# Performance work log

Measured on AMD Instinct MI355X. Metric: run time of the kernel, lower is better.

The kernel has to match this reference:

```python
import jax, jax.numpy as jnp
import numpy as np

L, N, E, H, D = 2048, 4, 1024, 16, 128  # seq, batch, embed, heads, proj_dim
HD = E // H                             # head_dim = 64
SIGMA = 1.0
EPS = 1e-6


def setup_inputs() -> dict:
    key = jax.random.key(0)
    ks = jax.random.split(key, 13)
    w = lambda i, shape: jax.random.normal(ks[i], shape, jnp.float32) * 0.02
    return {
        "query": jax.random.normal(ks[0], (L, N, E), jnp.float32),
        "key": jax.random.normal(ks[1], (L, N, E), jnp.float32),
        "value": jax.random.normal(ks[2], (L, N, E), jnp.float32),
        "wq": w(3, (E, E)), "bq": jnp.zeros((E,), jnp.float32),
        "wk": w(4, (E, E)), "bk": jnp.zeros((E,), jnp.float32),
        "wv": w(5, (E, E)), "bv": jnp.zeros((E,), jnp.float32),
        "wo": w(6, (E, E)), "bo": jnp.zeros((E,), jnp.float32),
        "random_matrices": SIGMA * jax.random.normal(ks[7], (H, D, HD), jnp.float32),
    }


def random_project(x, rm):
    # x: (L, N, H, HD), rm: (H, D, HD) -> phi: (N*H, L, 2D)
    scale = 1.0 / np.sqrt(2 * D).astype(np.float32)
    xn = x / jnp.maximum(jnp.linalg.norm(x, axis=-1, keepdims=True), 1e-12)
    xt = jnp.einsum('lnhe,hde->lnhd', xn, rm)
    phi = scale * jnp.concatenate([jnp.exp(xt), jnp.exp(-xt)], axis=-1)  # (L,N,H,2D)
    # faithful to torch .contiguous().view(-1, L, 2D): plain row-major reshape
    return phi.reshape(N * H, L, 2 * D)


def causal_product(phi_q, phi_k, v):
    # phi_q, phi_k: (B, L, 2D); v: (B, L, HD)
    B = phi_q.shape[0]
    def step(carry, inp):
        S, z = carry            # S: (B, 2D, HD) running kv; z: (B, 2D) running k-sum
        qk, kk, vv = inp        # (B, 2D), (B, 2D), (B, HD)
        S = S + kk[:, :, None] * vv[:, None, :]
        z = z + kk
        num = jnp.einsum('bd,bdh->bh', qk, S)
        den = jnp.einsum('bd,bd->b', qk, z)
        return (S, z), num / (den[:, None] + EPS)
    init = (jnp.zeros((B, 2 * D, HD), phi_q.dtype), jnp.zeros((B, 2 * D), phi_q.dtype))
    xs = (jnp.swapaxes(phi_q, 0, 1), jnp.swapaxes(phi_k, 0, 1), jnp.swapaxes(v, 0, 1))
    _, out = jax.lax.scan(step, init, xs)   # out: (L, B, HD)
    return jnp.swapaxes(out, 0, 1)          # (B, L, HD)


def reference(query, key, value, wq, bq, wk, bk, wv, bv, wo, bo, random_matrices):
    q = query @ wq.T + bq
    k = key @ wk.T + bk
    v = value @ wv.T + bv
    q = q.reshape(L, N, H, HD)
    k = k.reshape(L, N, H, HD)
    v = jnp.swapaxes(v.reshape(L, N * H, HD), 0, 1)   # (B=N*H, L, HD)
    phi_q = random_project(q, random_matrices)        # (B, L, 2D)
    phi_k = random_project(k, random_matrices)
    attn = causal_product(phi_q, phi_k, v)            # (B, L, HD)
    attn = jnp.swapaxes(attn, 0, 1).reshape(L, N, E)
    return attn @ wo.T + bo
```

## Files before the change

kernel.cpp:

```cpp
#include <hip/hip_runtime.h>
#include <math.h>


typedef unsigned short u16;
typedef unsigned int u32;
using f32x4v  = __attribute__((ext_vector_type(4))) float;
using f32x16v = __attribute__((ext_vector_type(16))) float;
using s16x8   = __attribute__((ext_vector_type(8))) short;

__device__ __forceinline__ float bf2f(u16 u) { return __uint_as_float(((u32)u) << 16); }
__device__ __forceinline__ u16 f2bf(float x) {
    u32 b = __float_as_uint(x);
    b += 0x7fff + ((b >> 16) & 1);
    return (u16)(b >> 16);
}
__device__ __forceinline__ u32 cvtpk(float lo, float hi) {
    u32 r;
    asm("v_cvt_pk_bf16_f32 %0, %1, %2" : "=v"(r) : "v"(lo), "v"(hi));
    return r;
}
__device__ __forceinline__ float exp2f_hw(float x) {
    float r;
    asm("v_exp_f32 %0, %1" : "=v"(r) : "v"(x));
    return r;
}
__device__ __forceinline__ void gload_lds16(const void* g, void* l) {
    __builtin_amdgcn_global_load_lds(
        (const __attribute__((address_space(1))) void*)g,
        (__attribute__((address_space(3))) void*)l, 16, 0, 0);
}

__global__ __launch_bounds__(256) void cvt_x_bf16(
    const float* __restrict__ q, const float* __restrict__ k,
    const float* __restrict__ v, u16* __restrict__ dst)
{
    const float* src = (blockIdx.y == 0) ? q : (blockIdx.y == 1) ? k : v;
    u16* d = dst + (size_t)blockIdx.y * 8388608;
    const size_t i = ((size_t)blockIdx.x * 256 + threadIdx.x) * 8;
    const float4 a = *(const float4*)(src + i);
    const float4 b = *(const float4*)(src + i + 4);
    u16 o[8] = {f2bf(a.x), f2bf(a.y), f2bf(a.z), f2bf(a.w),
                f2bf(b.x), f2bf(b.y), f2bf(b.z), f2bf(b.w)};
    *(uint4*)(d + i) = *(uint4*)o;
}

__global__ __launch_bounds__(256) void cvt_w_bf16(
    const float* __restrict__ w0, const float* __restrict__ w1,
    const float* __restrict__ w2, const float* __restrict__ w3,
    u16* __restrict__ dst)
{
    const float* src = (blockIdx.y == 0) ? w0 : (blockIdx.y == 1) ? w1
                     : (blockIdx.y == 2) ? w2 : w3;
    u16* d = dst + (size_t)blockIdx.y * 1048576;
    const size_t i = ((size_t)blockIdx.x * 256 + threadIdx.x) * 8;
    const float4 a = *(const float4*)(src + i);
    const float4 b = *(const float4*)(src + i + 4);
    u16 o[8] = {f2bf(a.x), f2bf(a.y), f2bf(a.z), f2bf(a.w),
                f2bf(b.x), f2bf(b.y), f2bf(b.z), f2bf(b.w)};
    *(uint4*)(d + i) = *(uint4*)o;
}

__global__ __launch_bounds__(256) void cvt_rm_bf16(
    const float* __restrict__ rm, u16* __restrict__ dst)
{
    const size_t i = ((size_t)blockIdx.x * 256 + threadIdx.x) * 8;
    const float4 a = *(const float4*)(rm + i);
    const float4 b = *(const float4*)(rm + i + 4);
    u16 o[8] = {f2bf(a.x), f2bf(a.y), f2bf(a.z), f2bf(a.w),
                f2bf(b.x), f2bf(b.y), f2bf(b.z), f2bf(b.w)};
    *(uint4*)(dst + i) = *(uint4*)o;
}

template<int OMODE>
__device__ __forceinline__ void gemm_body(
    const u16* __restrict__ A, const u16* __restrict__ Bw,
    const float* __restrict__ bias, void* __restrict__ Cp,
    int m0, int n0, u16* As, u16* Bs)
{
    const int t = threadIdx.x;
    const int wid = t >> 6, lane = t & 63;
    const int wr = wid >> 1, wc = wid & 1;
    const int l15 = lane & 15, l4 = lane >> 4;

    f32x4v acc[4][4];
#pragma unroll
    for (int i = 0; i < 4; ++i)
#pragma unroll
        for (int j = 0; j < 4; ++j)
#pragma unroll
            for (int e = 0; e < 4; ++e) acc[i][j][e] = 0.f;

    const int srow = wid * 32 + (lane >> 2);
    const int scol = (lane & 3) * 8;
    const u16* ga0 = A  + (size_t)(m0 + srow) * 1024 + scol;
    const u16* ga1 = ga0 + 16 * 1024;
    const u16* gb0 = Bw + (size_t)(n0 + srow) * 1024 + scol;
    const u16* gb1 = gb0 + 16 * 1024;
    u16* la0 = &As[wid * 1024];
    u16* la1 = la0 + 512;
    u16* lb0 = &Bs[wid * 1024];
    u16* lb1 = lb0 + 512;

    for (int k0 = 0; k0 < 1024; k0 += 32) {
        __syncthreads();
        gload_lds16(ga0 + k0, la0);
        gload_lds16(ga1 + k0, la1);
        gload_lds16(gb0 + k0, lb0);
        gload_lds16(gb1 + k0, lb1);
        __syncthreads();
        s16x8 af[4], bfr[4];
#pragma unroll
        for (int fi = 0; fi < 4; ++fi)
            af[fi] = *(const s16x8*)&As[(wr * 64 + fi * 16 + l15) * 32 + l4 * 8];
#pragma unroll
        for (int fj = 0; fj < 4; ++fj)
            bfr[fj] = *(const s16x8*)&Bs[(wc * 64 + fj * 16 + l15) * 32 + l4 * 8];
#pragma unroll
        for (int fi = 0; fi < 4; ++fi)
#pragma unroll
            for (int fj = 0; fj < 4; ++fj)
                acc[fi][fj] = __builtin_amdgcn_mfma_f32_16x16x32_bf16(af[fi], bfr[fj], acc[fi][fj], 0, 0, 0);
    }

    const int rl = l4 * 4, cl = l15;
    float bvals[4];
#pragma unroll
    for (int fj = 0; fj < 4; ++fj) bvals[fj] = bias[n0 + wc * 64 + fj * 16 + cl];
#pragma unroll
    for (int fi = 0; fi < 4; ++fi)
#pragma unroll
        for (int j = 0; j < 4; ++j) {
            const size_t m = m0 + wr * 64 + fi * 16 + rl + j;
#pragma unroll
            for (int fj = 0; fj < 4; ++fj) {
                const int n = n0 + wc * 64 + fj * 16 + cl;
                const float v = acc[fi][fj][j] + bvals[fj];
                if (OMODE == 0)      ((float*)Cp)[m * 1024 + n] = v;
                else if (OMODE == 1) ((u16*)Cp)[m * 1024 + n] = f2bf(v);
                else {
                    ((u16*)Cp)[((size_t)((m & 3) * 16 + (n >> 6)) * 64 + (n & 63)) * 2048 + (m >> 2)] = f2bf(v);
                }
            }
        }
}

template<int OMODE>
__global__ __launch_bounds__(256) void gemm_bf16(
    const u16* __restrict__ A, const u16* __restrict__ Bw,
    const float* __restrict__ bias, void* __restrict__ Cp)
{
    __shared__ __align__(16) u16 As[4096];
    __shared__ __align__(16) u16 Bs[4096];
    gemm_body<OMODE>(A, Bw, bias, Cp, blockIdx.x * 128, blockIdx.y * 128, As, Bs);
}

__global__ __launch_bounds__(256) void gemm_qk(
    const u16* __restrict__ xq, const u16* __restrict__ wq, const float* __restrict__ bq, u16* __restrict__ qp,
    const u16* __restrict__ xk, const u16* __restrict__ wk, const float* __restrict__ bk, u16* __restrict__ kp)
{
    __shared__ __align__(16) u16 As[4096];
    __shared__ __align__(16) u16 Bs[4096];
    const bool isq = (blockIdx.z == 0);
    gemm_body<1>(isq ? xq : xk, isq ? wq : wk, isq ? bq : bk, isq ? (void*)qp : (void*)kp,
                 blockIdx.x * 128, blockIdx.y * 128, As, Bs);
}

__global__ __launch_bounds__(256) void rand_project_mfma(
    const u16* __restrict__ QP, const u16* __restrict__ KP,
    const u16* __restrict__ RMB, u16* __restrict__ PHIQ, u16* __restrict__ PHIK)
{
    const u16* X  = (blockIdx.z == 0) ? QP : KP;
    u16* PHI      = (blockIdx.z == 0) ? PHIQ : PHIK;
    __shared__ __align__(16) u16 Xs[128 * 72];
    __shared__ __align__(16) u16 RMs[128 * 72];
    __shared__ float rsl_lds[128];
    const int h  = blockIdx.x;
    const int r0 = blockIdx.y * 128;
    const int t  = threadIdx.x;
    const int w  = t >> 6, lane = t & 63;
    const int l15 = lane & 15, l4 = lane >> 4;

    float sq[4];
#pragma unroll
    for (int i = 0; i < 4; ++i) {
        const int lin = t + i * 256;
        const int row = lin >> 3, oct = lin & 7;
        const uint4 xv = *(const uint4*)(X + (size_t)(r0 + row) * 1024 + h * 64 + oct * 8);
        *(uint4*)&Xs[row * 72 + oct * 8] = xv;
        const u16* pv = (const u16*)&xv;
        float s = 0.f;
#pragma unroll
        for (int e = 0; e < 8; ++e) { const float f = bf2f(pv[e]); s += f * f; }
        sq[i] = s;
        const uint4 rv = *(const uint4*)(RMB + (size_t)h * 8192 + lin * 8);
        *(uint4*)&RMs[row * 72 + oct * 8] = rv;
    }
#pragma unroll
    for (int i = 0; i < 4; ++i) {
        sq[i] += __shfl_xor(sq[i], 1);
        sq[i] += __shfl_xor(sq[i], 2);
        sq[i] += __shfl_xor(sq[i], 4);
        if ((t & 7) == 0)
            rsl_lds[(t >> 3) + i * 32] = 1.4426950408889634f / fmaxf(sqrtf(sq[i]), 1e-12f);
    }
    __syncthreads();

    const int wr = (w >> 1) * 64, wc = (w & 1) * 64;
    f32x4v acc[4][4];
#pragma unroll
    for (int i = 0; i < 4; ++i)
#pragma unroll
        for (int j = 0; j < 4; ++j)
#pragma unroll
            for (int e = 0; e < 4; ++e) acc[i][j][e] = 0.f;
#pragma unroll
    for (int ks = 0; ks < 2; ++ks) {
        s16x8 af[4], bfr[4];
#pragma unroll
        for (int fi = 0; fi < 4; ++fi)
            af[fi] = *(const s16x8*)&Xs[(wr + fi * 16 + l15) * 72 + ks * 32 + l4 * 8];
#pragma unroll
        for (int fj = 0; fj < 4; ++fj)
            bfr[fj] = *(const s16x8*)&RMs[(wc + fj * 16 + l15) * 72 + ks * 32 + l4 * 8];
#pragma unroll
        for (int fi = 0; fi < 4; ++fi)
#pragma unroll
            for (int fj = 0; fj < 4; ++fj)
                acc[fi][fj] = __builtin_amdgcn_mfma_f32_16x16x32_bf16(af[fi], bfr[fj], acc[fi][fj], 0, 0, 0);
    }

#pragma unroll
    for (int fi = 0; fi < 4; ++fi)
#pragma unroll
        for (int reg = 0; reg < 4; ++reg) {
            const int row = wr + fi * 16 + l4 * 4 + reg;
            const float rsl = rsl_lds[row];
            const size_t base = ((size_t)(r0 + row) * 16 + h) * 256;
#pragma unroll
            for (int fj = 0; fj < 4; ++fj) {
                const int d = wc + fj * 16 + l15;
                const float arg = acc[fi][fj][reg] * rsl;
                PHI[base + d]       = f2bf(exp2f_hw(arg - 4.f));
                PHI[base + 128 + d] = f2bf(exp2f_hw(-arg - 4.f));
            }
        }
}

__global__ __launch_bounds__(256) void chunk_state_mfma(
    const u16* __restrict__ PHIK, const u16* __restrict__ VPT, float* __restrict__ ST)
{
    __shared__ __align__(16) u16 Ks[64 * 136];
    __shared__ float zlds[16][132];
    const int b = blockIdx.x;
    const int c = blockIdx.y >> 1;
    const int dh = blockIdx.y & 1;
    const int t = threadIdx.x;
    const int wid = t >> 6, lane = t & 63;
    const int l15 = lane & 15, l4 = lane >> 4;
    const int wr = wid >> 1, wc = wid & 1;

    const size_t R0 = (size_t)b * 2048 + (size_t)c * 256;
    const int rgrp = t >> 4, d08 = (t & 15) * 8;

    float zpart[8];
#pragma unroll
    for (int i = 0; i < 8; ++i) zpart[i] = 0.f;

    f32x4v acc[2][4];
#pragma unroll
    for (int i = 0; i < 2; ++i)
#pragma unroll
        for (int j = 0; j < 4; ++j)
#pragma unroll
            for (int e = 0; e < 4; ++e) acc[i][j][e] = 0.f;

    for (int stage = 0; stage < 4; ++stage) {
        __syncthreads();
#pragma unroll
        for (int j = 0; j < 4; ++j) {
            const int r = rgrp + 16 * j;
            const uint4 v = *(const uint4*)(PHIK + (R0 + stage * 64 + r) * 256 + dh * 128 + d08);
            const int x = ((r >> 3) & 3) << 1;
            *(uint4*)&Ks[r * 136 + (((d08 >> 3) ^ x) << 3)] = v;
            const u16* pv = (const u16*)&v;
#pragma unroll
            for (int i = 0; i < 8; ++i) zpart[i] += bf2f(pv[i]);
        }
        __syncthreads();
#pragma unroll
        for (int ks = 0; ks < 2; ++ks) {
            const int xk = ((ks * 4 + l4) & 3) << 1;
            const int r0 = ks * 32 + l4 * 8;
            s16x8 af[2], bk[4];
#pragma unroll
            for (int fi = 0; fi < 2; ++fi) {
                const int h = wr * 32 + fi * 16 + l15;
                af[fi] = *(const s16x8*)(VPT + ((size_t)b * 64 + h) * 2048 + c * 256 + stage * 64 + ks * 32 + l4 * 8);
            }
#pragma unroll
            for (int fj = 0; fj < 4; ++fj) {
                const int d = wc * 64 + fj * 16 + l15;
                const int colk = (((d >> 3) ^ xk) << 3) + (d & 7);
#pragma unroll
                for (int e = 0; e < 8; ++e)
                    bk[fj][e] = (short)Ks[(r0 + e) * 136 + colk];
            }
#pragma unroll
            for (int fi = 0; fi < 2; ++fi)
#pragma unroll
                for (int fj = 0; fj < 4; ++fj)
                    acc[fi][fj] = __builtin_amdgcn_mfma_f32_16x16x32_bf16(af[fi], bk[fj], acc[fi][fj], 0, 0, 0);
        }
    }
    __syncthreads();
    *(float4*)&zlds[rgrp][d08]     = *(float4*)&zpart[0];
    *(float4*)&zlds[rgrp][d08 + 4] = *(float4*)&zpart[4];
    __syncthreads();
    float* st = ST + (size_t)(b * 8 + c) * 16640;
    if (t < 128) {
        float z = 0.f;
#pragma unroll
        for (int g = 0; g < 16; ++g) z += zlds[g][t];
        st[16384 + dh * 128 + t] = z;
    }
#pragma unroll
    for (int fi = 0; fi < 2; ++fi)
#pragma unroll
        for (int reg = 0; reg < 4; ++reg) {
            const int h = wr * 32 + fi * 16 + l4 * 4 + reg;
#pragma unroll
            for (int fj = 0; fj < 4; ++fj) {
                const int d = dh * 128 + wc * 64 + fj * 16 + l15;
                st[(size_t)h * 256 + d] = acc[fi][fj][reg];
            }
        }
}

__global__ void prefix_scan(const float* __restrict__ ST, u16* __restrict__ STBF)
{
    const int b = blockIdx.x;
    const int e = blockIdx.y * 256 + threadIdx.x;
    if (e >= 16640) return;
    const size_t base = (size_t)b * 8 * 16640 + e;
    float run = 0.f;
#pragma unroll
    for (int c = 0; c < 8; ++c) {
        const float v = ST[base + (size_t)c * 16640];
        STBF[(size_t)(b * 8 + c) * 16640 + e] = f2bf(run);
        run += v;
    }
}

__global__ __launch_bounds__(128) void causal_fused(
    const u16* __restrict__ PHIQ, const u16* __restrict__ PHIK,
    const u16* __restrict__ VPT, const u16* __restrict__ STBF,
    u16* __restrict__ ATT)
{
    const u32 bid = blockIdx.x;
    const int pair = (int)((bid >> 3) & 3);
    const int G  = (int)((bid >> 5) * 8 + (bid & 7));
    const int b  = G & 63;
    const int c  = G >> 6;
    const int w  = threadIdx.x >> 6;
    const int rf = w ? (7 - pair) : pair;
    const int ri = rf >> 1, fi = rf & 1;
    const int lane = threadIdx.x & 63;
    const int l31 = lane & 31, s = lane >> 5;
    const size_t chunk0 = (size_t)b * 2048 + (size_t)c * 256;
    const u16* stb = STBF + (size_t)(b * 8 + c) * 16640;

    const int qc = ri * 64 + fi * 32 + l31;
    s16x8 qf[16];
    const u16* qp = PHIQ + (chunk0 + qc) * 256 + s * 8;
#pragma unroll
    for (int ds = 0; ds < 16; ++ds)
        qf[ds] = *(const s16x8*)(qp + ds * 16);

    f32x16v o[2], o2;
#pragma unroll
    for (int e = 0; e < 16; ++e) { o[0][e] = 0.f; o[1][e] = 0.f; o2[e] = 0.f; }
    float den = 0.f;

#pragma unroll
    for (int ds = 0; ds < 16; ++ds) {
        const s16x8 zf = *(const s16x8*)(stb + 16384 + ds * 16 + s * 8);
        o2 = __builtin_amdgcn_mfma_f32_32x32x16_bf16(qf[ds], zf, o2, 0, 0, 0);
#pragma unroll
        for (int fh = 0; fh < 2; ++fh) {
            const s16x8 sx = *(const s16x8*)(stb + (fh * 32 + l31) * 256 + ds * 16 + s * 8);
            o[fh] = __builtin_amdgcn_mfma_f32_32x32x16_bf16(qf[ds], sx, o[fh], 0, 0, 0);
        }
    }

    const int kbmax = ri * 2 + fi;
    for (int kb = 0; kb <= kbmax; ++kb) {
        s16x8 vf[2][2];
#pragma unroll
        for (int kh = 0; kh < 2; ++kh)
#pragma unroll
            for (int fh = 0; fh < 2; ++fh)
                vf[kh][fh] = *(const s16x8*)(VPT + ((size_t)b * 64 + fh * 32 + l31) * 2048
                                             + c * 256 + kb * 32 + kh * 16 + s * 8);
        f32x16v p0, p1;
#pragma unroll
        for (int e = 0; e < 16; ++e) { p0[e] = 0.f; p1[e] = 0.f; }
        const u16* kptr = PHIK + (chunk0 + kb * 32 + l31) * 256 + s * 8;
#pragma unroll
        for (int ds = 0; ds < 8; ++ds) {
            const s16x8 kf0 = *(const s16x8*)(kptr + (2 * ds) * 16);
            const s16x8 kf1 = *(const s16x8*)(kptr + (2 * ds + 1) * 16);
            p0 = __builtin_amdgcn_mfma_f32_32x32x16_bf16(kf0, qf[2 * ds],     p0, 0, 0, 0);
            p1 = __builtin_amdgcn_mfma_f32_32x32x16_bf16(kf1, qf[2 * ds + 1], p1, 0, 0, 0);
        }
        f32x16v p;
#pragma unroll
        for (int e = 0; e < 16; ++e) p[e] = p0[e] + p1[e];

        const bool diag = (kb == kbmax);
        float rsum = 0.f;
#pragma unroll
        for (int reg = 0; reg < 16; ++reg) {
            if (diag) {
                const int kc = kb * 32 + (reg & 3) + 8 * (reg >> 2) + 4 * s;
                if (kc > qc) p[reg] = 0.f;
            }
            rsum += p[reg];
        }
        den += rsum;
#pragma unroll
        for (int kh = 0; kh < 2; ++kh) {
            const u32 pA_lo = cvtpk(p[8*kh + 0], p[8*kh + 1]);
            const u32 pA_hi = cvtpk(p[8*kh + 2], p[8*kh + 3]);
            const u32 pB_lo = cvtpk(p[8*kh + 4], p[8*kh + 5]);
            const u32 pB_hi = cvtpk(p[8*kh + 6], p[8*kh + 7]);
            const u32 X_lo = s ? pB_lo : pA_lo;
            const u32 X_hi = s ? pB_hi : pA_hi;
            const u32 Y_lo = s ? pA_lo : pB_lo;
            const u32 Y_hi = s ? pA_hi : pB_hi;
            const u32 sY_lo = __shfl_xor((int)Y_lo, 32);
            const u32 sY_hi = __shfl_xor((int)Y_hi, 32);
            u32 wq[4];
            wq[0] = s ? sY_lo : X_lo;
            wq[1] = s ? sY_hi : X_hi;
            wq[2] = s ? X_lo : sY_lo;
            wq[3] = s ? X_hi : sY_hi;
            s16x8 pa;
#pragma unroll
            for (int i = 0; i < 4; ++i) {
                pa[2*i]   = (short)(wq[i] & 0xffff);
                pa[2*i+1] = (short)(wq[i] >> 16);
            }
            o[0] = __builtin_amdgcn_mfma_f32_32x32x16_bf16(pa, vf[kh][0], o[0], 0, 0, 0);
            o[1] = __builtin_amdgcn_mfma_f32_32x32x16_bf16(pa, vf[kh][1], o[1], 0, 0, 0);
        }
    }

    const float denT = den + __shfl_xor(den, 32);
#pragma unroll
    for (int reg = 0; reg < 16; ++reg) {
        const int q32 = (reg & 3) + 8 * (reg >> 2) + 4 * s;
        const float dv = o2[reg] + __shfl(denT, q32);
        const float inv = 1.f / (dv + 1e-6f);
        const int qrow = c * 256 + ri * 64 + fi * 32 + q32;
        const size_t abase = (size_t)qrow * 4096 + b * 64;
        ATT[abase + l31]      = f2bf(o[0][reg] * inv);
        ATT[abase + 32 + l31] = f2bf(o[1][reg] * inv);
    }
}

extern "C" void kernel_launch(void* const* d_in, const int* in_sizes, int n_in,
                              void* d_out, int out_size, void* d_ws, size_t ws_size,
                              hipStream_t stream)
{
    const float* query = (const float*)d_in[0];
    const float* key   = (const float*)d_in[1];
    const float* value = (const float*)d_in[2];
    const float* wq    = (const float*)d_in[3];
    const float* bq    = (const float*)d_in[4];
    const float* wk    = (const float*)d_in[5];
    const float* bk    = (const float*)d_in[6];
    const float* wv    = (const float*)d_in[7];
    const float* bv    = (const float*)d_in[8];
    const float* wo    = (const float*)d_in[9];
    const float* bo    = (const float*)d_in[10];
    const float* rm    = (const float*)d_in[11];
    float* out = (float*)d_out;

    char* base = (char*)d_ws;
    u16*   phiq = (u16*)(base);
    u16*   phik = (u16*)(base +  67108864);
    u16*   qp   = (u16*)(base + 134217728);
    u16*   vpt  = (u16*)(base + 134217728);
    u16*   kp   = (u16*)(base + 150994944);
    u16*   stbf = (u16*)(base + 150994944);
    u16*   xbf  = (u16*)(base + 168034304);
    float* st   = (float*)(base + 168034304);
    u16*   attn = (u16*)(base + 168034304);
    u16*   wbf  = (u16*)(base + 218365952);
    u16*   rmb  = (u16*)(base + 226754560);

    u16* xq = xbf;
    u16* xk = xbf +  8388608;
    u16* xv = xbf + 16777216;
    u16* wqb = wbf;
    u16* wkb = wbf + 1048576;
    u16* wvb = wbf + 2097152;
    u16* wob = wbf + 3145728;

    const dim3 blk(256);
    cvt_x_bf16<<<dim3(4096, 3), blk, 0, stream>>>(query, key, value, xbf);
    cvt_w_bf16<<<dim3(512, 4), blk, 0, stream>>>(wq, wk, wv, wo, wbf);
    cvt_rm_bf16<<<dim3(64), blk, 0, stream>>>(rm, rmb);
    gemm_qk<<<dim3(64, 8, 2), blk, 0, stream>>>(xq, wqb, bq, qp, xk, wkb, bk, kp);
    rand_project_mfma<<<dim3(16, 64, 2), blk, 0, stream>>>(qp, kp, rmb, phiq, phik);
    gemm_bf16<2><<<dim3(64, 8), blk, 0, stream>>>(xv, wvb, bv, vpt);
    chunk_state_mfma<<<dim3(64, 16), blk, 0, stream>>>(phik, vpt, st);
    prefix_scan<<<dim3(64, 65), blk, 0, stream>>>(st, stbf);
    causal_fused<<<dim3(2048), dim3(128), 0, stream>>>(phiq, phik, vpt, stbf, attn);
    gemm_bf16<0><<<dim3(64, 8), blk, 0, stream>>>(attn, wob, bo, out);
}
```

Before: 291.3 us.

## Fuse input bf16 conversion into QKV GEMM and specialize causal intra-chunk loop

Drops the separate fp32-to-bf16 pass over the activations. The merged Q/K/V projection GEMM now reads fp32 inputs, converts them in registers and stores them to a swizzled LDS tile, and the V projection joins the same launch. The weight and random-matrix conversions are merged into one launch. Chunk states are stored as bf16 instead of fp32 to halve prefix-scan traffic, at some cost in precision. The causal kernel templates its intra-chunk loop on the block count so it fully unrolls, adds s_setprio around the MFMA sections, and sets a waves-per-EU launch bound.

```diff
diff --git a/kernel.cpp b/kernel.cpp
--- a/kernel.cpp
+++ b/kernel.cpp
@@ -30,12 +30,21 @@
         (__attribute__((address_space(3))) void*)l, 16, 0, 0);
 }
 
-__global__ __launch_bounds__(256) void cvt_x_bf16(
-    const float* __restrict__ q, const float* __restrict__ k,
-    const float* __restrict__ v, u16* __restrict__ dst)
-{
-    const float* src = (blockIdx.y == 0) ? q : (blockIdx.y == 1) ? k : v;
-    u16* d = dst + (size_t)blockIdx.y * 8388608;
+__global__ __launch_bounds__(256) void cvt_consts(
+    const float* __restrict__ w0, const float* __restrict__ w1,
+    const float* __restrict__ w2, const float* __restrict__ w3,
+    const float* __restrict__ rm, u16* __restrict__ wbf, u16* __restrict__ rmb)
+{
+    const int y = blockIdx.y;
+    const float* src;
+    u16* d;
+    if (y == 4) {
+        if (blockIdx.x >= 64) return;
+        src = rm; d = rmb;
+    } else {
+        src = (y == 0) ? w0 : (y == 1) ? w1 : (y == 2) ? w2 : w3;
+        d = wbf + (size_t)y * 1048576;
+    }
     const size_t i = ((size_t)blockIdx.x * 256 + threadIdx.x) * 8;
     const float4 a = *(const float4*)(src + i);
     const float4 b = *(const float4*)(src + i + 4);
@@ -44,40 +53,107 @@
     *(uint4*)(d + i) = *(uint4*)o;
 }
 
-__global__ __launch_bounds__(256) void cvt_w_bf16(
-    const float* __restrict__ w0, const float* __restrict__ w1,
-    const float* __restrict__ w2, const float* __restrict__ w3,
-    u16* __restrict__ dst)
-{
-    const float* src = (blockIdx.y == 0) ? w0 : (blockIdx.y == 1) ? w1
-                     : (blockIdx.y == 2) ? w2 : w3;
-    u16* d = dst + (size_t)blockIdx.y * 1048576;
-    const size_t i = ((size_t)blockIdx.x * 256 + threadIdx.x) * 8;
-    const float4 a = *(const float4*)(src + i);
-    const float4 b = *(const float4*)(src + i + 4);
-    u16 o[8] = {f2bf(a.x), f2bf(a.y), f2bf(a.z), f2bf(a.w),
-                f2bf(b.x), f2bf(b.y), f2bf(b.z), f2bf(b.w)};
-    *(uint4*)(d + i) = *(uint4*)o;
-}
-
-__global__ __launch_bounds__(256) void cvt_rm_bf16(
-    const float* __restrict__ rm, u16* __restrict__ dst)
-{
-    const size_t i = ((size_t)blockIdx.x * 256 + threadIdx.x) * 8;
-    const float4 a = *(const float4*)(rm + i);
-    const float4 b = *(const float4*)(rm + i + 4);
-    u16 o[8] = {f2bf(a.x), f2bf(a.y), f2bf(a.z), f2bf(a.w),
-                f2bf(b.x), f2bf(b.y), f2bf(b.z), f2bf(b.w)};
-    *(uint4*)(dst + i) = *(uint4*)o;
-}
-
-template<int OMODE>
-__device__ __forceinline__ void gemm_body(
+__global__ __launch_bounds__(256) void gemm_qkv(
+    const float* __restrict__ Xq, const float* __restrict__ Xk, const float* __restrict__ Xv,
+    const u16* __restrict__ WB, const float* __restrict__ bq, const float* __restrict__ bk,
+    const float* __restrict__ bv, u16* __restrict__ qp, u16* __restrict__ kp, u16* __restrict__ vpt)
+{
+    __shared__ __align__(16) u16 As[4096];
+    __shared__ __align__(16) u16 Bs[4096];
+    const int z = blockIdx.z;
+    const float* A = (z == 0) ? Xq : (z == 1) ? Xk : Xv;
+    const u16* Bw = WB + (size_t)z * 1048576;
+    const float* bias = (z == 0) ? bq : (z == 1) ? bk : bv;
+
+    const int t = threadIdx.x;
+    const int m0 = blockIdx.x * 128, n0 = blockIdx.y * 128;
+    const int wid = t >> 6, lane = t & 63;
+    const int wr = wid >> 1, wc = wid & 1;
+    const int l15 = lane & 15, l4 = lane >> 4;
+
+    f32x4v acc[4][4];
+#pragma unroll
+    for (int i = 0; i < 4; ++i)
+#pragma unroll
+        for (int j = 0; j < 4; ++j)
+#pragma unroll
+            for (int e = 0; e < 4; ++e) acc[i][j][e] = 0.f;
+
+    const int srow = t >> 1;
+    const int scol = (t & 1) * 16;
+    const int sx   = (srow >> 1) & 3;
+    const int sl0  = (t & 1) * 2;
+    u16* wa0 = &As[srow * 32 + ((sl0     ^ sx)) * 8];
+    u16* wa1 = &As[srow * 32 + (((sl0+1) ^ sx)) * 8];
+    const float* gsrcA = A + (size_t)(m0 + srow) * 1024 + scol;
+    const int brow = wid * 32 + (lane >> 2);
+    const int bcol = (lane & 3) * 8;
+    const u16* gb0 = Bw + (size_t)(n0 + brow) * 1024 + bcol;
+    const u16* gb1 = gb0 + 16 * 1024;
+    u16* lb0 = &Bs[wid * 1024];
+    u16* lb1 = lb0 + 512;
+
+    for (int k0 = 0; k0 < 1024; k0 += 32) {
+        __syncthreads();
+        gload_lds16(gb0 + k0, lb0);
+        gload_lds16(gb1 + k0, lb1);
+        {
+            u16 ta[16];
+#pragma unroll
+            for (int q = 0; q < 4; ++q) {
+                const float4 v = *(const float4*)(gsrcA + k0 + q * 4);
+                ta[q*4+0] = f2bf(v.x); ta[q*4+1] = f2bf(v.y);
+                ta[q*4+2] = f2bf(v.z); ta[q*4+3] = f2bf(v.w);
+            }
+            *(uint4*)wa0 = *(const uint4*)&ta[0];
+            *(uint4*)wa1 = *(const uint4*)&ta[8];
+        }
+        __syncthreads();
+        s16x8 af[4], bfr[4];
+#pragma unroll
+        for (int fi = 0; fi < 4; ++fi) {
+            const int r  = wr * 64 + fi * 16 + l15;
+            const int sl = l4 ^ ((r >> 1) & 3);
+            af[fi] = *(const s16x8*)&As[r * 32 + sl * 8];
+        }
+#pragma unroll
+        for (int fj = 0; fj < 4; ++fj)
+            bfr[fj] = *(const s16x8*)&Bs[(wc * 64 + fj * 16 + l15) * 32 + l4 * 8];
+#pragma unroll
+        for (int fi = 0; fi < 4; ++fi)
+#pragma unroll
+            for (int fj = 0; fj < 4; ++fj)
+                acc[fi][fj] = __builtin_amdgcn_mfma_f32_16x16x32_bf16(af[fi], bfr[fj], acc[fi][fj], 0, 0, 0);
+    }
+
+    u16* Cp = (z == 0) ? qp : (z == 1) ? kp : vpt;
+    const int rl = l4 * 4, cl = l15;
+    float bvals[4];
+#pragma unroll
+    for (int fj = 0; fj < 4; ++fj) bvals[fj] = bias[n0 + wc * 64 + fj * 16 + cl];
+#pragma unroll
+    for (int fi = 0; fi < 4; ++fi)
+#pragma unroll
+        for (int j = 0; j < 4; ++j) {
+            const size_t m = m0 + wr * 64 + fi * 16 + rl + j;
+#pragma unroll
+            for (int fj = 0; fj < 4; ++fj) {
+                const int n = n0 + wc * 64 + fj * 16 + cl;
+                const float v = acc[fi][fj][j] + bvals[fj];
+                if (z < 2) Cp[m * 1024 + n] = f2bf(v);
+                else       Cp[((size_t)((m & 3) * 16 + (n >> 6)) * 64 + (n & 63)) * 2048 + (m >> 2)] = f2bf(v);
+            }
+        }
+}
+
+__global__ __launch_bounds__(256) void gemm_o(
     const u16* __restrict__ A, const u16* __restrict__ Bw,
-    const float* __restrict__ bias, void* __restrict__ Cp,
-    int m0, int n0, u16* As, u16* Bs)
-{
+    const float* __restrict__ bias, float* __restrict__ Cp)
+{
+    __shared__ __align__(16) u16 As[4096];
+    __shared__ __align__(16) u16 Bs[4096];
     const int t = threadIdx.x;
+    const int m0 = blockIdx.x * 128, n0 = blockIdx.y * 128;
     const int wid = t >> 6, lane = t & 63;
     const int wr = wid >> 1, wc = wid & 1;
     const int l15 = lane & 15, l4 = lane >> 4;
@@ -134,35 +210,9 @@
 #pragma unroll
             for (int fj = 0; fj < 4; ++fj) {
                 const int n = n0 + wc * 64 + fj * 16 + cl;
-                const float v = acc[fi][fj][j] + bvals[fj];
-                if (OMODE == 0)      ((float*)Cp)[m * 1024 + n] = v;
-                else if (OMODE == 1) ((u16*)Cp)[m * 1024 + n] = f2bf(v);
-                else {
-                    ((u16*)Cp)[((size_t)((m & 3) * 16 + (n >> 6)) * 64 + (n & 63)) * 2048 + (m >> 2)] = f2bf(v);
-                }
-            }
-        }
-}
-
-template<int OMODE>
-__global__ __launch_bounds__(256) void gemm_bf16(
-    const u16* __restrict__ A, const u16* __restrict__ Bw,
-    const float* __restrict__ bias, void* __restrict__ Cp)
-{
-    __shared__ __align__(16) u16 As[4096];
-    __shared__ __align__(16) u16 Bs[4096];
-    gemm_body<OMODE>(A, Bw, bias, Cp, blockIdx.x * 128, blockIdx.y * 128, As, Bs);
-}
-
-__global__ __launch_bounds__(256) void gemm_qk(
-    const u16* __restrict__ xq, const u16* __restrict__ wq, const float* __restrict__ bq, u16* __restrict__ qp,
-    const u16* __restrict__ xk, const u16* __restrict__ wk, const float* __restrict__ bk, u16* __restrict__ kp)
-{
-    __shared__ __align__(16) u16 As[4096];
-    __shared__ __align__(16) u16 Bs[4096];
-    const bool isq = (blockIdx.z == 0);
-    gemm_body<1>(isq ? xq : xk, isq ? wq : wk, isq ? bq : bk, isq ? (void*)qp : (void*)kp,
-                 blockIdx.x * 128, blockIdx.y * 128, As, Bs);
+                Cp[m * 1024 + n] = acc[fi][fj][j] + bvals[fj];
+            }
+        }
 }
 
 __global__ __launch_bounds__(256) void rand_project_mfma(
@@ -247,7 +297,7 @@
 }
 
 __global__ __launch_bounds__(256) void chunk_state_mfma(
-    const u16* __restrict__ PHIK, const u16* __restrict__ VPT, float* __restrict__ ST)
+    const u16* __restrict__ PHIK, const u16* __restrict__ VPT, u16* __restrict__ STC)
 {
     __shared__ __align__(16) u16 Ks[64 * 136];
     __shared__ float zlds[16][132];
@@ -316,12 +366,12 @@
     *(float4*)&zlds[rgrp][d08]     = *(float4*)&zpart[0];
     *(float4*)&zlds[rgrp][d08 + 4] = *(float4*)&zpart[4];
     __syncthreads();
-    float* st = ST + (size_t)(b * 8 + c) * 16640;
+    u16* st = STC + (size_t)(b * 8 + c) * 16640;
     if (t < 128) {
         float z = 0.f;
 #pragma unroll
         for (int g = 0; g < 16; ++g) z += zlds[g][t];
-        st[16384 + dh * 128 + t] = z;
+        st[16384 + dh * 128 + t] = f2bf(z);
     }
 #pragma unroll
     for (int fi = 0; fi < 2; ++fi)
@@ -331,80 +381,46 @@
 #pragma unroll
             for (int fj = 0; fj < 4; ++fj) {
                 const int d = dh * 128 + wc * 64 + fj * 16 + l15;
-                st[(size_t)h * 256 + d] = acc[fi][fj][reg];
-            }
-        }
-}
-
-__global__ void prefix_scan(const float* __restrict__ ST, u16* __restrict__ STBF)
+                st[(size_t)h * 256 + d] = f2bf(acc[fi][fj][reg]);
+            }
+        }
+}
+
+__global__ void prefix_scan(const u16* __restrict__ STC, u16* __restrict__ STBF)
 {
     const int b = blockIdx.x;
     const int e = blockIdx.y * 256 + threadIdx.x;
     if (e >= 16640) return;
-    const size_t base = (size_t)b * 8 * 16640 + e;
     float run = 0.f;
 #pragma unroll
     for (int c = 0; c < 8; ++c) {
-        const float v = ST[base + (size_t)c * 16640];
-        STBF[(size_t)(b * 8 + c) * 16640 + e] = f2bf(run);
+        const size_t idx = (size_t)(b * 8 + c) * 16640 + e;
+        const float v = bf2f(STC[idx]);
+        STBF[idx] = f2bf(run);
         run += v;
     }
 }
 
-__global__ __launch_bounds__(128) void causal_fused(
-    const u16* __restrict__ PHIQ, const u16* __restrict__ PHIK,
-    const u16* __restrict__ VPT, const u16* __restrict__ STBF,
-    u16* __restrict__ ATT)
-{
-    const u32 bid = blockIdx.x;
-    const int pair = (int)((bid >> 3) & 3);
-    const int G  = (int)((bid >> 5) * 8 + (bid & 7));
-    const int b  = G & 63;
-    const int c  = G >> 6;
-    const int w  = threadIdx.x >> 6;
-    const int rf = w ? (7 - pair) : pair;
-    const int ri = rf >> 1, fi = rf & 1;
-    const int lane = threadIdx.x & 63;
-    const int l31 = lane & 31, s = lane >> 5;
-    const size_t chunk0 = (size_t)b * 2048 + (size_t)c * 256;
-    const u16* stb = STBF + (size_t)(b * 8 + c) * 16640;
-
-    const int qc = ri * 64 + fi * 32 + l31;
-    s16x8 qf[16];
-    const u16* qp = PHIQ + (chunk0 + qc) * 256 + s * 8;
-#pragma unroll
-    for (int ds = 0; ds < 16; ++ds)
-        qf[ds] = *(const s16x8*)(qp + ds * 16);
-
-    f32x16v o[2], o2;
-#pragma unroll
-    for (int e = 0; e < 16; ++e) { o[0][e] = 0.f; o[1][e] = 0.f; o2[e] = 0.f; }
-    float den = 0.f;
-
-#pragma unroll
-    for (int ds = 0; ds < 16; ++ds) {
-        const s16x8 zf = *(const s16x8*)(stb + 16384 + ds * 16 + s * 8);
-        o2 = __builtin_amdgcn_mfma_f32_32x32x16_bf16(qf[ds], zf, o2, 0, 0, 0);
-#pragma unroll
-        for (int fh = 0; fh < 2; ++fh) {
-            const s16x8 sx = *(const s16x8*)(stb + (fh * 32 + l31) * 256 + ds * 16 + s * 8);
-            o[fh] = __builtin_amdgcn_mfma_f32_32x32x16_bf16(qf[ds], sx, o[fh], 0, 0, 0);
-        }
-    }
-
-    const int kbmax = ri * 2 + fi;
-    for (int kb = 0; kb <= kbmax; ++kb) {
+template<int KBMAX>
+__device__ __forceinline__ void intra_unit(
+    const u16* __restrict__ kbase, const u16* __restrict__ vbase,
+    const s16x8 (&qf)[16], int qc, int l31, int s,
+    f32x16v& o0, f32x16v& o1, float& den)
+{
+#pragma unroll
+    for (int kb = 0; kb <= KBMAX; ++kb) {
         s16x8 vf[2][2];
 #pragma unroll
         for (int kh = 0; kh < 2; ++kh)
 #pragma unroll
             for (int fh = 0; fh < 2; ++fh)
-                vf[kh][fh] = *(const s16x8*)(VPT + ((size_t)b * 64 + fh * 32 + l31) * 2048
-                                             + c * 256 + kb * 32 + kh * 16 + s * 8);
+                vf[kh][fh] = *(const s16x8*)(vbase + (size_t)(fh * 32 + l31) * 2048
+                                             + kb * 32 + kh * 16 + s * 8);
         f32x16v p0, p1;
 #pragma unroll
         for (int e = 0; e < 16; ++e) { p0[e] = 0.f; p1[e] = 0.f; }
-        const u16* kptr = PHIK + (chunk0 + kb * 32 + l31) * 256 + s * 8;
+        const u16* kptr = kbase + (size_t)(kb * 32 + l31) * 256 + s * 8;
+        __builtin_amdgcn_s_setprio(1);
 #pragma unroll
         for (int ds = 0; ds < 8; ++ds) {
             const s16x8 kf0 = *(const s16x8*)(kptr + (2 * ds) * 16);
@@ -412,11 +428,12 @@
             p0 = __builtin_amdgcn_mfma_f32_32x32x16_bf16(kf0, qf[2 * ds],     p0, 0, 0, 0);
             p1 = __builtin_amdgcn_mfma_f32_32x32x16_bf16(kf1, qf[2 * ds + 1], p1, 0, 0, 0);
         }
+        __builtin_amdgcn_s_setprio(0);
         f32x16v p;
 #pragma unroll
         for (int e = 0; e < 16; ++e) p[e] = p0[e] + p1[e];
 
-        const bool diag = (kb == kbmax);
+        const bool diag = (kb == KBMAX);
         float rsum = 0.f;
 #pragma unroll
         for (int reg = 0; reg < 16; ++reg) {
@@ -450,9 +467,67 @@
                 pa[2*i]   = (short)(wq[i] & 0xffff);
                 pa[2*i+1] = (short)(wq[i] >> 16);
             }
-            o[0] = __builtin_amdgcn_mfma_f32_32x32x16_bf16(pa, vf[kh][0], o[0], 0, 0, 0);
-            o[1] = __builtin_amdgcn_mfma_f32_32x32x16_bf16(pa, vf[kh][1], o[1], 0, 0, 0);
-        }
+            __builtin_amdgcn_s_setprio(1);
+            o0 = __builtin_amdgcn_mfma_f32_32x32x16_bf16(pa, vf[kh][0], o0, 0, 0, 0);
+            o1 = __builtin_amdgcn_mfma_f32_32x32x16_bf16(pa, vf[kh][1], o1, 0, 0, 0);
+            __builtin_amdgcn_s_setprio(0);
+        }
+    }
+}
+
+__global__ __launch_bounds__(128, 3) void causal_fused(
+    const u16* __restrict__ PHIQ, const u16* __restrict__ PHIK,
+    const u16* __restrict__ VPT, const u16* __restrict__ STBF,
+    u16* __restrict__ ATT)
+{
+    const u32 bid = blockIdx.x;
+    const int pair = (int)((bid >> 3) & 3);
+    const int G  = (int)((bid >> 5) * 8 + (bid & 7));
+    const int b  = G & 63;
+    const int c  = G >> 6;
+    const int w  = threadIdx.x >> 6;
+    const int rf = w ? (7 - pair) : pair;
+    const int ri = rf >> 1, fi = rf & 1;
+    const int lane = threadIdx.x & 63;
+    const int l31 = lane & 31, s = lane >> 5;
+    const size_t chunk0 = (size_t)b * 2048 + (size_t)c * 256;
+    const u16* stb = STBF + (size_t)(b * 8 + c) * 16640;
+
+    const int qc = ri * 64 + fi * 32 + l31;
+    s16x8 qf[16];
+    const u16* qp = PHIQ + (chunk0 + qc) * 256 + s * 8;
+#pragma unroll
+    for (int ds = 0; ds < 16; ++ds)
+        qf[ds] = *(const s16x8*)(qp + ds * 16);
+
+    f32x16v o[2], o2;
+#pragma unroll
+    for (int e = 0; e < 16; ++e) { o[0][e] = 0.f; o[1][e] = 0.f; o2[e] = 0.f; }
+    float den = 0.f;
+
+#pragma unroll
+    for (int ds = 0; ds < 16; ++ds) {
+        const s16x8 zf = *(const s16x8*)(stb + 16384 + ds * 16 + s * 8);
+        o2 = __builtin_amdgcn_mfma_f32_32x32x16_bf16(qf[ds], zf, o2, 0, 0, 0);
+#pragma unroll
+        for (int fh = 0; fh < 2; ++fh) {
+            const s16x8 sx = *(const s16x8*)(stb + (fh * 32 + l31) * 256 + ds * 16 + s * 8);
+            o[fh] = __builtin_amdgcn_mfma_f32_32x32x16_bf16(qf[ds], sx, o[fh], 0, 0, 0);
+        }
+    }
+
+    const u16* kbase = PHIK + chunk0 * 256;
+    const u16* vbase = VPT + (size_t)b * 64 * 2048 + c * 256;
+    const int kbmax = ri * 2 + fi;
+    switch (kbmax) {
+        case 0: intra_unit<0>(kbase, vbase, qf, qc, l31, s, o[0], o[1], den); break;
+        case 1: intra_unit<1>(kbase, vbase, qf, qc, l31, s, o[0], o[1], den); break;
+        case 2: intra_unit<2>(kbase, vbase, qf, qc, l31, s, o[0], o[1], den); break;
+        case 3: intra_unit<3>(kbase, vbase, qf, qc, l31, s, o[0], o[1], den); break;
+        case 4: intra_unit<4>(kbase, vbase, qf, qc, l31, s, o[0], o[1], den); break;
+        case 5: intra_unit<5>(kbase, vbase, qf, qc, l31, s, o[0], o[1], den); break;
+        case 6: intra_unit<6>(kbase, vbase, qf, qc, l31, s, o[0], o[1], den); break;
+        default: intra_unit<7>(kbase, vbase, qf, qc, l31, s, o[0], o[1], den); break;
     }
 
     const float denT = den + __shfl_xor(den, 32);
@@ -487,35 +562,28 @@
     float* out = (float*)d_out;
 
     char* base = (char*)d_ws;
-    u16*   phiq = (u16*)(base);
-    u16*   phik = (u16*)(base +  67108864);
-    u16*   qp   = (u16*)(base + 134217728);
-    u16*   vpt  = (u16*)(base + 134217728);
-    u16*   kp   = (u16*)(base + 150994944);
-    u16*   stbf = (u16*)(base + 150994944);
-    u16*   xbf  = (u16*)(base + 168034304);
-    float* st   = (float*)(base + 168034304);
-    u16*   attn = (u16*)(base + 168034304);
-    u16*   wbf  = (u16*)(base + 218365952);
-    u16*   rmb  = (u16*)(base + 226754560);
-
-    u16* xq = xbf;
-    u16* xk = xbf +  8388608;
-    u16* xv = xbf + 16777216;
+    u16* phiq = (u16*)(base);
+    u16* phik = (u16*)(base +  67108864);
+    u16* vpt  = (u16*)(base + 134217728);
+    u16* stbf = (u16*)(base + 150994944);
+    u16* qp   = (u16*)(base + 168034304);
+    u16* kp   = (u16*)(base + 184811520);
+    u16* stc  = (u16*)(base + 201588736);
+    u16* wbf  = (u16*)(base + 218628096);
+    u16* rmb  = (u16*)(base + 227016704);
+    u16* attn = qp;
+
     u16* wqb = wbf;
     u16* wkb = wbf + 1048576;
     u16* wvb = wbf + 2097152;
     u16* wob = wbf + 3145728;
 
     const dim3 blk(256);
-    cvt_x_bf16<<<dim3(4096, 3), blk, 0, stream>>>(query, key, value, xbf);
-    cvt_w_bf16<<<dim3(512, 4), blk, 0, stream>>>(wq, wk, wv, wo, wbf);
-    cvt_rm_bf16<<<dim3(64), blk, 0, stream>>>(rm, rmb);
-    gemm_qk<<<dim3(64, 8, 2), blk, 0, stream>>>(xq, wqb, bq, qp, xk, wkb, bk, kp);
+    cvt_consts<<<dim3(512, 5), blk, 0, stream>>>(wq, wk, wv, wo, rm, wbf, rmb);
+    gemm_qkv<<<dim3(64, 8, 3), blk, 0, stream>>>(query, key, value, wbf, bq, bk, bv, qp, kp, vpt);
     rand_project_mfma<<<dim3(16, 64, 2), blk, 0, stream>>>(qp, kp, rmb, phiq, phik);
-    gemm_bf16<2><<<dim3(64, 8), blk, 0, stream>>>(xv, wvb, bv, vpt);
-    chunk_state_mfma<<<dim3(64, 16), blk, 0, stream>>>(phik, vpt, st);
-    prefix_scan<<<dim3(64, 65), blk, 0, stream>>>(st, stbf);
+    chunk_state_mfma<<<dim3(64, 16), blk, 0, stream>>>(phik, vpt, stc);
+    prefix_scan<<<dim3(64, 65), blk, 0, stream>>>(stc, stbf);
     causal_fused<<<dim3(2048), dim3(128), 0, stream>>>(phiq, phik, vpt, stbf, attn);
-    gemm_bf16<0><<<dim3(64, 8), blk, 0, stream>>>(attn, wob, bo, out);
-}
+    gemm_o<<<dim3(64, 8), blk, 0, stream>>>(attn, wob, bo, out);
+}
```

After: 377.3 us. 1.3x slower.
